# Kernel tuning notes

Hardware: AMD Instinct MI355X
Metric: run time of the kernel (lower is better)

## Reference

```python
import jax, jax.numpy as jnp
import numpy as np

H = 128
W = 128
DELTA = 7000.0  # sigmainv in the original (delta default 7000)


def setup_inputs() -> dict:
    key = jax.random.key(0)
    k1, k2, k3, k4 = jax.random.split(key, 4)
    B, P, F, TH, TW = 2, 300, 512, 512, 512
    points_bxpx3 = jax.random.uniform(k1, (B, P, 3), jnp.float32) * 2.0 - 1.0  # NDC cube [-1,1]
    faces_fx3 = jax.random.randint(k2, (F, 3), 0, P, dtype=jnp.int32)
    uv_bxpx2 = jax.random.uniform(k3, (B, P, 2), jnp.float32)  # texcoords in [0,1]
    texture_bx3xthxtw = jax.random.uniform(k4, (B, 3, TH, TW), jnp.float32)
    return {"points_bxpx3": points_bxpx3, "faces_fx3": faces_fx3,
            "uv_bxpx2": uv_bxpx2, "texture_bx3xthxtw": texture_bx3xthxtw}


def _edge(ax, ay, bx, by, px, py):
    # signed area * 2 of triangle (a, b, p); standard edge function
    return (bx - ax) * (py - ay) - (by - ay) * (px - ax)


def _seg_d2(ax, ay, bx, by, px, py):
    # squared distance from point p to segment (a, b)
    abx, aby = bx - ax, by - ay
    apx, apy = px - ax, py - ay
    denom = abx * abx + aby * aby + 1e-12
    t = jnp.clip((apx * abx + apy * aby) / denom, 0.0, 1.0)
    dx = apx - t * abx
    dy = apy - t * aby
    return dx * dx + dy * dy


def _rasterize(points_bxpx3, faces_fx3, feats_bxfx3xd, height, width, delta):
    """Soft DIB-R-style rasterizer.
    Returns (imfeat [B,H,W,D], improb [B,H,W,1]).
    """
    B = points_bxpx3.shape[0]
    v = points_bxpx3[:, faces_fx3]                      # (B,F,3,3) gathered face vertices
    x0, x1, x2 = (v[:, :, i, 0][:, :, None, None] for i in range(3))
    y0, y1, y2 = (v[:, :, i, 1][:, :, None, None] for i in range(3))
    z0, z1, z2 = (v[:, :, i, 2][:, :, None, None] for i in range(3))

    # pixel-center grid in NDC; y flipped (top row = +1)
    px = ((jnp.arange(width, dtype=points_bxpx3.dtype) + 0.5) / width * 2.0 - 1.0)[None, None, None, :]
    py = (1.0 - (jnp.arange(height, dtype=points_bxpx3.dtype) + 0.5) / height * 2.0)[None, None, :, None]

    area = _edge(x0, y0, x1, y1, x2, y2)                # (B,F,1,1) == normal_z (cross-product z)
    front = area > 1e-8                                  # front-facing (normalz > 0) cull
    inv_area = 1.0 / jnp.where(front, area, 1.0)

    w0 = _edge(x1, y1, x2, y2, px, py) * inv_area        # (B,F,H,W) barycentrics
    w1 = _edge(x2, y2, x0, y0, px, py) * inv_area
    w2 = _edge(x0, y0, x1, y1, px, py) * inv_area
    inside = front & (w0 >= 0) & (w1 >= 0) & (w2 >= 0)

    z_pix = w0 * z0 + w1 * z1 + w2 * z2                  # interpolated depth
    zbuf = jnp.where(inside, z_pix, -1e9)
    best = jnp.argmax(zbuf, axis=1)                      # (B,H,W) nearest covering face
    hit = jnp.any(inside, axis=1)[..., None].astype(points_bxpx3.dtype)  # (B,H,W,1)

    # gather winning barycentrics and per-face vertex features
    w = jnp.stack([w0, w1, w2], axis=-1)                 # (B,F,H,W,3)
    idx = jnp.broadcast_to(best[:, None, :, :, None], (B, 1, height, width, 3))
    wb = jnp.take_along_axis(w, idx, axis=1)[:, 0]       # (B,H,W,3)
    fb = jax.vmap(lambda f, i: f[i])(feats_bxfx3xd, best)  # (B,H,W,3,D)
    imfeat = jnp.einsum('bhwk,bhwkd->bhwd', wb, fb) * hit

    # soft coverage: prob of each face = exp(-delta * d2(pixel, triangle)); z-buffer blend
    d2 = jnp.minimum(
        jnp.minimum(_seg_d2(x0, y0, x1, y1, px, py), _seg_d2(x1, y1, x2, y2, px, py)),
        _seg_d2(x2, y2, x0, y0, px, py))
    d2 = jnp.where(inside, 0.0, d2)
    p = jnp.where(front, jnp.exp(-delta * d2), 0.0)      # (B,F,H,W)
    log_miss = jnp.sum(jnp.log1p(-jnp.clip(p, 0.0, 1.0 - 1e-7)), axis=1)  # (B,H,W)
    improb = (1.0 - jnp.exp(log_miss))[..., None]
    return imfeat, improb


def _fragmentshader(imtexcoords, texture_bx3xthxtw, hardmask):
    # bilinear texture sampling; background is zero
    B, C, TH, TW = texture_bx3xthxtw.shape
    u = jnp.clip(imtexcoords[..., 0], 0.0, 1.0)
    vv = jnp.clip(imtexcoords[..., 1], 0.0, 1.0)
    fx = u * (TW - 1)
    fy = (1.0 - vv) * (TH - 1)
    x0 = jnp.floor(fx).astype(jnp.int32); x1 = jnp.minimum(x0 + 1, TW - 1)
    y0 = jnp.floor(fy).astype(jnp.int32); y1 = jnp.minimum(y0 + 1, TH - 1)
    wx = (fx - x0)[:, None]; wy = (fy - y0)[:, None]     # (B,1,H,W)

    def g(tex, yy, xx):  # tex (C,TH,TW), yy/xx (H,W) -> (C,H,W)
        return tex[:, yy, xx]
    c00 = jax.vmap(g)(texture_bx3xthxtw, y0, x0)
    c01 = jax.vmap(g)(texture_bx3xthxtw, y0, x1)
    c10 = jax.vmap(g)(texture_bx3xthxtw, y1, x0)
    c11 = jax.vmap(g)(texture_bx3xthxtw, y1, x1)
    col = (c00 * (1 - wx) * (1 - wy) + c01 * wx * (1 - wy)
           + c10 * (1 - wx) * wy + c11 * wx * wy)        # (B,C,H,W)
    return col.transpose(0, 2, 3, 1) * hardmask          # (B,H,W,C)


def reference(points_bxpx3, faces_fx3, uv_bxpx2, texture_bx3xthxtw):
    # texture mode: per-face vertex features = [u, v, mask=1]
    uvf = uv_bxpx2[:, faces_fx3]                          # (B,F,3,2)
    ones = jnp.ones_like(uvf[..., :1])
    feats = jnp.concatenate([uvf, ones], axis=-1)         # (B,F,3,3)
    imfeat, improb = _rasterize(points_bxpx3, faces_fx3, feats, H, W, DELTA)
    imtexcoords = imfeat[..., :2]
    hardmask = jax.lax.stop_gradient(imfeat[..., 2:3])    # .detach() in the original
    imrender = _fragmentshader(imtexcoords, texture_bx3xthxtw, hardmask)
    return imrender, improb
```

## Files before the change

kernel.cpp:

```cpp
#include <hip/hip_runtime.h>
#include <math.h>

constexpr int kB = 2, kP = 300, kF = 512, kH = 128, kW = 128, kTH = 512, kTW = 512;
constexpr float kDelta = 7000.0f;
constexpr float kCut = 0.06f;
constexpr float kThr2 = 0.018882f;
constexpr float kLogInside = -15.9423847f;

__global__ __launch_bounds__(512, 6) void render_all(const float* __restrict__ pts,
                                                     const int* __restrict__ faces,
                                                     const float* __restrict__ uvs,
                                                     const float* __restrict__ tex,
                                                     float* __restrict__ out) {
    __shared__ float4 sA[kF], sB[kF], sC[kF];
    __shared__ float2 s_vtx[kF * 3];
    __shared__ unsigned short s_of[kF];
    __shared__ int s_wsum[8];
    __shared__ float s_bz[512];
    __shared__ int s_bi[512];
    __shared__ float s_lm[512];

    int tile = (int)blockIdx.x;
    int b = tile >> 8;
    int rem = tile & 255;
    int ty = rem >> 4, tx = rem & 15;
    int tid = (int)threadIdx.x;
    int lane = tid & 63;
    int wv = tid >> 6;

    {
        int f = tid;
        int i0 = faces[f * 3 + 0], i1 = faces[f * 3 + 1], i2 = faces[f * 3 + 2];
        const float* pb = pts + b * kP * 3;
        float x0 = pb[i0 * 3], y0 = pb[i0 * 3 + 1], z0 = pb[i0 * 3 + 2];
        float x1 = pb[i1 * 3], y1 = pb[i1 * 3 + 1], z1 = pb[i1 * 3 + 2];
        float x2 = pb[i2 * 3], y2 = pb[i2 * 3 + 1], z2 = pb[i2 * 3 + 2];
        float area = (x1 - x0) * (y2 - y0) - (y1 - y0) * (x2 - x0);
        bool front = area > 1e-8f;

        sA[f] = make_float4(0.0f, 0.0f, -1e30f, 0.0f);
        sB[f] = make_float4(0.0f, -1e30f, 0.0f, 0.0f);
        sC[f] = make_float4(-1e30f, 0.0f, 0.0f, 0.0f);
        s_vtx[f * 3 + 0] = make_float2(1e15f, 1e15f);
        s_vtx[f * 3 + 1] = make_float2(1e15f, 1e15f);
        s_vtx[f * 3 + 2] = make_float2(1e15f, 1e15f);
        unsigned long long bal = __ballot(front);
        if (lane == 0) s_wsum[wv] = __popcll(bal);
        __syncthreads();

        int base = 0;
#pragma unroll
        for (int w = 0; w < 8; ++w) base += (w < wv) ? s_wsum[w] : 0;
        int k = base + __popcll(bal & ((1ull << lane) - 1ull));

        if (front) {
            int slot = ((k & 7) << 6) | (k >> 3);
            float inv_a = 1.0f / area;
            float e0x = x2 - x1, e0y = y2 - y1;
            float e1x = x0 - x2, e1y = y0 - y2;
            float e2x = x1 - x0, e2y = y1 - y0;
            float l0 = fmaf(e0x, e0x, e0y * e0y);
            float l1 = fmaf(e1x, e1x, e1y * e1y);
            float l2 = fmaf(e2x, e2x, e2y * e2y);
            float s0 = rsqrtf(l0 + 1e-12f);
            float s1 = rsqrtf(l1 + 1e-12f);
            float s2 = rsqrtf(l2 + 1e-12f);
            float A0 = -e0y * s0, B0 = e0x * s0, C0 = (e0y * x1 - e0x * y1) * s0;
            float A1 = -e1y * s1, B1 = e1x * s1, C1 = (e1y * x2 - e1x * y2) * s1;
            float A2 = -e2y * s2, B2 = e2x * s2, C2 = (e2y * x0 - e2x * y0) * s2;
            float a0 = -e0y * inv_a, b0 = e0x * inv_a, c0 = (e0y * x1 - e0x * y1) * inv_a;
            float a1 = -e1y * inv_a, b1 = e1x * inv_a, c1 = (e1y * x2 - e1x * y2) * inv_a;
            float a2 = -e2y * inv_a, b2 = e2x * inv_a, c2 = (e2y * x0 - e2x * y0) * inv_a;
            sA[slot] = make_float4(A0, B0, C0, A1);
            sB[slot] = make_float4(B1, C1, A2, B2);
            sC[slot] = make_float4(C2,
                                   a0 * z0 + a1 * z1 + a2 * z2,
                                   b0 * z0 + b1 * z1 + b2 * z2,
                                   c0 * z0 + c1 * z1 + c2 * z2);
            s_vtx[slot * 3 + 0] = make_float2(x0, y0);
            s_vtx[slot * 3 + 1] = make_float2(x1, y1);
            s_vtx[slot * 3 + 2] = make_float2(x2, y2);
            s_of[slot] = (unsigned short)f;
        }
    }
    __syncthreads();

    int pyi = ty * 8 + (lane >> 3);
    int pxi = tx * 8 + (lane & 7);
    float px = ((float)pxi + 0.5f) * (2.0f / 128.0f) - 1.0f;
    float py = 1.0f - ((float)pyi + 0.5f) * (2.0f / 128.0f);

    float cx = (float)(tx * 8 + 4) * (2.0f / 128.0f) - 1.0f;
    float cy = 1.0f - (float)(ty * 8 + 4) * (2.0f / 128.0f);
    unsigned long long m;
    {
        int slt = (wv << 6) + lane;
        float4 a4 = sA[slt];
        float4 b4 = sB[slt];
        float4 c4 = sC[slt];
        float L0 = fmaf(a4.x, cx, fmaf(a4.y, cy, a4.z));
        float L1 = fmaf(a4.w, cx, fmaf(b4.x, cy, b4.y));
        float L2 = fmaf(b4.z, cx, fmaf(b4.w, cy, c4.x));
        float minc = fminf(fminf(L0, L1), L2);
        float2 v0 = s_vtx[slt * 3 + 0];
        float2 v1 = s_vtx[slt * 3 + 1];
        float2 v2 = s_vtx[slt * 3 + 2];
        float e0x = v2.x - v1.x, e0y = v2.y - v1.y;
        float e1x = v0.x - v2.x, e1y = v0.y - v2.y;
        float e2x = v1.x - v0.x, e2y = v1.y - v0.y;
        float p0x = cx - v0.x, p0y = cy - v0.y;
        float p1x = cx - v1.x, p1y = cy - v1.y;
        float p2x = cx - v2.x, p2y = cy - v2.y;
        float dot0 = fmaf(p1x, e0x, p1y * e0y), len0 = fmaf(e0x, e0x, e0y * e0y);
        float dot1 = fmaf(p2x, e1x, p2y * e1y), len1 = fmaf(e1x, e1x, e1y * e1y);
        float dot2 = fmaf(p0x, e2x, p0y * e2y), len2 = fmaf(e2x, e2x, e2y * e2y);
        float c0 = (dot0 >= 0.0f && dot0 <= len0) ? L0 * L0 : 1e30f;
        float c1 = (dot1 >= 0.0f && dot1 <= len1) ? L1 * L1 : 1e30f;
        float c2 = (dot2 >= 0.0f && dot2 <= len2) ? L2 * L2 : 1e30f;
        float dv0 = fmaf(p0x, p0x, p0y * p0y);
        float dv1 = fmaf(p1x, p1x, p1y * p1y);
        float dv2 = fmaf(p2x, p2x, p2y * p2y);
        float d2c = fminf(fminf(fminf(c0, c1), fminf(c2, dv0)), fminf(dv1, dv2));
        bool admit = (minc >= 0.0f) | (d2c <= kThr2);
        m = __ballot(admit);
    }

    float bestz = -1e9f;
    int besti = -1, icnt = 0;
    float lm = 0.0f;

    while (m) {
        int l = (int)__builtin_ctzll(m);
        m &= (m - 1);
        int fs = (wv << 6) + l;
        int k = (l << 3) | wv;
        float4 h0 = sA[fs];
        float4 h1 = sB[fs];
        float4 h2 = sC[fs];
        float L0 = fmaf(h0.x, px, fmaf(h0.y, py, h0.z));
        float L1 = fmaf(h0.w, px, fmaf(h1.x, py, h1.y));
        float L2 = fmaf(h1.z, px, fmaf(h1.w, py, h2.x));
        float minL = fminf(fminf(L0, L1), L2);
        bool inside = minL >= 0.0f;
        float z = fmaf(h2.y, px, fmaf(h2.z, py, h2.w));
        if (inside && z > bestz) { bestz = z; besti = k; }
        icnt += inside ? 1 : 0;
        float db = fminf(fminf(fabsf(L0), fabsf(L1)), fabsf(L2));
        bool need = (!inside) & (db < kCut);
        if (__any(need)) {
            float2 v0 = s_vtx[fs * 3 + 0];
            float2 v1 = s_vtx[fs * 3 + 1];
            float2 v2 = s_vtx[fs * 3 + 2];
            float e0x = v2.x - v1.x, e0y = v2.y - v1.y;
            float e1x = v0.x - v2.x, e1y = v0.y - v2.y;
            float e2x = v1.x - v0.x, e2y = v1.y - v0.y;
            float p0x = px - v0.x, p0y = py - v0.y;
            float p1x = px - v1.x, p1y = py - v1.y;
            float p2x = px - v2.x, p2y = py - v2.y;
            float dot0 = fmaf(p1x, e0x, p1y * e0y), len0 = fmaf(e0x, e0x, e0y * e0y);
            float dot1 = fmaf(p2x, e1x, p2y * e1y), len1 = fmaf(e1x, e1x, e1y * e1y);
            float dot2 = fmaf(p0x, e2x, p0y * e2y), len2 = fmaf(e2x, e2x, e2y * e2y);
            float c0 = (dot0 >= 0.0f && dot0 <= len0) ? L0 * L0 : 1e30f;
            float c1 = (dot1 >= 0.0f && dot1 <= len1) ? L1 * L1 : 1e30f;
            float c2 = (dot2 >= 0.0f && dot2 <= len2) ? L2 * L2 : 1e30f;
            float dv0 = fmaf(p0x, p0x, p0y * p0y);
            float dv1 = fmaf(p1x, p1x, p1y * p1y);
            float dv2 = fmaf(p2x, p2x, p2y * p2y);
            float d2 = fminf(fminf(fminf(c0, c1), fminf(c2, dv0)), fminf(dv1, dv2));
            float p = __expf(-kDelta * d2);
            p = fminf(p, 1.0f - 1e-7f);
            float lp = __logf(1.0f - p);
            lm += need ? lp : 0.0f;
        }
    }
    lm = fmaf((float)icnt, kLogInside, lm);

    s_bz[tid] = bestz;
    s_bi[tid] = besti;
    s_lm[tid] = lm;
    __syncthreads();

    if (tid < 64) {
        float bz = s_bz[tid];
        int bi = s_bi[tid];
        float L = s_lm[tid];
#pragma unroll
        for (int w = 1; w < 8; ++w) {
            float z2 = s_bz[w * 64 + tid];
            int ii = s_bi[w * 64 + tid];
            L += s_lm[w * 64 + tid];
            if (z2 > bz || (z2 == bz && ii >= 0 && (unsigned)ii < (unsigned)bi)) {
                bz = z2; bi = ii;
            }
        }
        float improb = 1.0f - expf(L);
        float u = 0.0f, v = 0.0f, mk = 0.0f;
        if (bi >= 0) {
            int slot = ((bi & 7) << 6) | (bi >> 3);
            float2 v0 = s_vtx[slot * 3 + 0];
            float2 v1 = s_vtx[slot * 3 + 1];
            float2 v2 = s_vtx[slot * 3 + 2];
            float area = (v1.x - v0.x) * (v2.y - v0.y) - (v1.y - v0.y) * (v2.x - v0.x);
            float inv_a = 1.0f / area;
            float w0 = ((v2.x - v1.x) * (py - v1.y) - (v2.y - v1.y) * (px - v1.x)) * inv_a;
            float w1 = ((v0.x - v2.x) * (py - v2.y) - (v0.y - v2.y) * (px - v2.x)) * inv_a;
            float w2 = ((v1.x - v0.x) * (py - v0.y) - (v1.y - v0.y) * (px - v0.x)) * inv_a;
            int of = (int)s_of[slot];
            int j0 = faces[of * 3], j1 = faces[of * 3 + 1], j2 = faces[of * 3 + 2];
            const float* ub = uvs + b * kP * 2;
            u = w0 * ub[j0 * 2] + w1 * ub[j1 * 2] + w2 * ub[j2 * 2];
            v = w0 * ub[j0 * 2 + 1] + w1 * ub[j1 * 2 + 1] + w2 * ub[j2 * 2 + 1];
            mk = w0 + w1 + w2;
        }
        float uc = fminf(fmaxf(u, 0.0f), 1.0f);
        float vc = fminf(fmaxf(v, 0.0f), 1.0f);
        float fx = uc * (float)(kTW - 1);
        float fy = (1.0f - vc) * (float)(kTH - 1);
        int xi0 = (int)floorf(fx), yi0 = (int)floorf(fy);
        int xi1 = min(xi0 + 1, kTW - 1), yi1 = min(yi0 + 1, kTH - 1);
        float wx = fx - (float)xi0, wy = fy - (float)yi0;
        float w00 = (1.0f - wx) * (1.0f - wy);
        float w01 = wx * (1.0f - wy);
        float w10 = (1.0f - wx) * wy;
        float w11 = wx * wy;
        int o00 = yi0 * kTW + xi0, o01 = yi0 * kTW + xi1;
        int o10 = yi1 * kTW + xi0, o11 = yi1 * kTW + xi1;
        const float* tb = tex + (size_t)b * 3 * kTH * kTW;
        float cols[3];
#pragma unroll
        for (int c = 0; c < 3; ++c) {
            const float* tc = tb + c * kTH * kTW;
            cols[c] = (tc[o00] * w00 + tc[o01] * w01 + tc[o10] * w10 + tc[o11] * w11) * mk;
        }
        int pix = (b * kH + pyi) * kW + pxi;
        out[pix * 3 + 0] = cols[0];
        out[pix * 3 + 1] = cols[1];
        out[pix * 3 + 2] = cols[2];
        out[kB * kH * kW * 3 + pix] = improb;
    }
}

extern "C" void kernel_launch(void* const* d_in, const int* in_sizes, int n_in,
                              void* d_out, int out_size, void* d_ws, size_t ws_size,
                              hipStream_t stream) {
    const float* pts = (const float*)d_in[0];
    const int* faces = (const int*)d_in[1];
    const float* uvs = (const float*)d_in[2];
    const float* tex = (const float*)d_in[3];
    float* out = (float*)d_out;
    render_all<<<kB * 256, 512, 0, stream>>>(pts, faces, uvs, tex, out);
}
```

Baseline: 18.32 us.

## Split face setup into a prep kernel and stage precomputed face data via workspace

Per-face edge and depth-plane setup, plus the gathered UVs, now runs once per batch in a small prep kernel that writes a compacted table to workspace. Each render block copies that table into shared memory with coalesced float4 loads instead of redoing the gather and setup in all 512 blocks, and the final shading reads UVs from shared memory rather than global. The cull thresholds are also tightened, which admits fewer faces and reduces soft-probability work but changes the approximation margin. In exchange it adds a second launch with a dependency, and the larger shared footprint is aliased for the reduction, which needs an extra barrier.

Result: slower. 21.76 us (+18.8%).

```diff
diff --git a/kernel.cpp b/kernel.cpp
--- a/kernel.cpp
+++ b/kernel.cpp
@@ -3,22 +3,94 @@
 
 constexpr int kB = 2, kP = 300, kF = 512, kH = 128, kW = 128, kTH = 512, kTW = 512;
 constexpr float kDelta = 7000.0f;
-constexpr float kCut = 0.06f;
-constexpr float kThr2 = 0.018882f;
+constexpr float kCut = 0.0363f;
+constexpr float kThr2 = 0.012928f;
 constexpr float kLogInside = -15.9423847f;
-
-__global__ __launch_bounds__(512, 6) void render_all(const float* __restrict__ pts,
-                                                     const int* __restrict__ faces,
-                                                     const float* __restrict__ uvs,
-                                                     const float* __restrict__ tex,
-                                                     float* __restrict__ out) {
-    __shared__ float4 sA[kF], sB[kF], sC[kF];
-    __shared__ float2 s_vtx[kF * 3];
-    __shared__ unsigned short s_of[kF];
+constexpr int kS4 = 3072;
+
+__global__ __launch_bounds__(512) void prep(const float* __restrict__ pts,
+                                            const int* __restrict__ faces,
+                                            const float* __restrict__ uvs,
+                                            float4* __restrict__ ws4) {
+    int b = (int)blockIdx.x;
+    int tid = (int)threadIdx.x, lane = tid & 63, wv = tid >> 6;
     __shared__ int s_wsum[8];
-    __shared__ float s_bz[512];
-    __shared__ int s_bi[512];
-    __shared__ float s_lm[512];
+
+    int f = tid;
+    int i0 = faces[f * 3 + 0], i1 = faces[f * 3 + 1], i2 = faces[f * 3 + 2];
+    const float* pb = pts + b * kP * 3;
+    float x0 = pb[i0 * 3], y0 = pb[i0 * 3 + 1], z0 = pb[i0 * 3 + 2];
+    float x1 = pb[i1 * 3], y1 = pb[i1 * 3 + 1], z1 = pb[i1 * 3 + 2];
+    float x2 = pb[i2 * 3], y2 = pb[i2 * 3 + 1], z2 = pb[i2 * 3 + 2];
+    float area = (x1 - x0) * (y2 - y0) - (y1 - y0) * (x2 - x0);
+    bool front = area > 1e-8f;
+
+    unsigned long long bal = __ballot(front);
+    if (lane == 0) s_wsum[wv] = __popcll(bal);
+    __syncthreads();
+    int n = 0, base = 0;
+#pragma unroll
+    for (int w = 0; w < 8; ++w) { n += s_wsum[w]; base += (w < wv) ? s_wsum[w] : 0; }
+    int k = base + __popcll(bal & ((1ull << lane) - 1ull));
+
+    float4* A = ws4 + (size_t)b * kS4;
+    float4* B = A + 512;
+    float4* C = B + 512;
+    float4* V = C + 512;
+    float4* U = V + 1024;
+
+    if (tid >= n) {
+        int s = ((tid & 7) << 6) | (tid >> 3);
+        A[s] = make_float4(0.0f, 0.0f, -1e30f, 0.0f);
+        B[s] = make_float4(0.0f, -1e30f, 0.0f, 0.0f);
+        C[s] = make_float4(-1e30f, 0.0f, 0.0f, 0.0f);
+        V[s * 2 + 0] = make_float4(1e15f, 1e15f, 1e15f, 1e15f);
+        V[s * 2 + 1] = make_float4(1e15f, 1e15f, 0.0f, 0.0f);
+        U[s] = make_float4(0.0f, 0.0f, 0.0f, 0.0f);
+    }
+    if (front) {
+        int s = ((k & 7) << 6) | (k >> 3);
+        float inv_a = 1.0f / area;
+        float e0x = x2 - x1, e0y = y2 - y1;
+        float e1x = x0 - x2, e1y = y0 - y2;
+        float e2x = x1 - x0, e2y = y1 - y0;
+        float l0 = fmaf(e0x, e0x, e0y * e0y);
+        float l1 = fmaf(e1x, e1x, e1y * e1y);
+        float l2 = fmaf(e2x, e2x, e2y * e2y);
+        float s0 = rsqrtf(l0 + 1e-12f);
+        float s1 = rsqrtf(l1 + 1e-12f);
+        float s2 = rsqrtf(l2 + 1e-12f);
+        float A0 = -e0y * s0, B0 = e0x * s0, C0 = (e0y * x1 - e0x * y1) * s0;
+        float A1 = -e1y * s1, B1 = e1x * s1, C1 = (e1y * x2 - e1x * y2) * s1;
+        float A2 = -e2y * s2, B2 = e2x * s2, C2 = (e2y * x0 - e2x * y0) * s2;
+        float a0 = -e0y * inv_a, b0 = e0x * inv_a, c0 = (e0y * x1 - e0x * y1) * inv_a;
+        float a1 = -e1y * inv_a, b1 = e1x * inv_a, c1 = (e1y * x2 - e1x * y2) * inv_a;
+        float a2 = -e2y * inv_a, b2 = e2x * inv_a, c2 = (e2y * x0 - e2x * y0) * inv_a;
+        A[s] = make_float4(A0, B0, C0, A1);
+        B[s] = make_float4(B1, C1, A2, B2);
+        C[s] = make_float4(C2,
+                           a0 * z0 + a1 * z1 + a2 * z2,
+                           b0 * z0 + b1 * z1 + b2 * z2,
+                           c0 * z0 + c1 * z1 + c2 * z2);
+        const float* ub = uvs + b * kP * 2;
+        V[s * 2 + 0] = make_float4(x0, y0, x1, y1);
+        V[s * 2 + 1] = make_float4(x2, y2, ub[i0 * 2], ub[i0 * 2 + 1]);
+        U[s] = make_float4(ub[i1 * 2], ub[i1 * 2 + 1], ub[i2 * 2], ub[i2 * 2 + 1]);
+    }
+}
+
+__global__ __launch_bounds__(512, 6) void render(const float4* __restrict__ ws4,
+                                                 const float* __restrict__ tex,
+                                                 float* __restrict__ out) {
+    __shared__ float4 s_all[kS4];
+    float4* sA = s_all;
+    float4* sB = s_all + 512;
+    float4* sC = s_all + 1024;
+    float4* sV = s_all + 1536;
+    float4* sU = s_all + 2560;
+    float* s_bz = (float*)s_all;
+    int* s_bi = (int*)((char*)s_all + 2048);
+    float* s_lm = (float*)((char*)s_all + 4096);
 
     int tile = (int)blockIdx.x;
     int b = tile >> 8;
@@ -29,59 +101,8 @@
     int wv = tid >> 6;
 
     {
-        int f = tid;
-        int i0 = faces[f * 3 + 0], i1 = faces[f * 3 + 1], i2 = faces[f * 3 + 2];
-        const float* pb = pts + b * kP * 3;
-        float x0 = pb[i0 * 3], y0 = pb[i0 * 3 + 1], z0 = pb[i0 * 3 + 2];
-        float x1 = pb[i1 * 3], y1 = pb[i1 * 3 + 1], z1 = pb[i1 * 3 + 2];
-        float x2 = pb[i2 * 3], y2 = pb[i2 * 3 + 1], z2 = pb[i2 * 3 + 2];
-        float area = (x1 - x0) * (y2 - y0) - (y1 - y0) * (x2 - x0);
-        bool front = area > 1e-8f;
-
-        sA[f] = make_float4(0.0f, 0.0f, -1e30f, 0.0f);
-        sB[f] = make_float4(0.0f, -1e30f, 0.0f, 0.0f);
-        sC[f] = make_float4(-1e30f, 0.0f, 0.0f, 0.0f);
-        s_vtx[f * 3 + 0] = make_float2(1e15f, 1e15f);
-        s_vtx[f * 3 + 1] = make_float2(1e15f, 1e15f);
-        s_vtx[f * 3 + 2] = make_float2(1e15f, 1e15f);
-        unsigned long long bal = __ballot(front);
-        if (lane == 0) s_wsum[wv] = __popcll(bal);
-        __syncthreads();
-
-        int base = 0;
-#pragma unroll
-        for (int w = 0; w < 8; ++w) base += (w < wv) ? s_wsum[w] : 0;
-        int k = base + __popcll(bal & ((1ull << lane) - 1ull));
-
-        if (front) {
-            int slot = ((k & 7) << 6) | (k >> 3);
-            float inv_a = 1.0f / area;
-            float e0x = x2 - x1, e0y = y2 - y1;
-            float e1x = x0 - x2, e1y = y0 - y2;
-            float e2x = x1 - x0, e2y = y1 - y0;
-            float l0 = fmaf(e0x, e0x, e0y * e0y);
-            float l1 = fmaf(e1x, e1x, e1y * e1y);
-            float l2 = fmaf(e2x, e2x, e2y * e2y);
-            float s0 = rsqrtf(l0 + 1e-12f);
-            float s1 = rsqrtf(l1 + 1e-12f);
-            float s2 = rsqrtf(l2 + 1e-12f);
-            float A0 = -e0y * s0, B0 = e0x * s0, C0 = (e0y * x1 - e0x * y1) * s0;
-            float A1 = -e1y * s1, B1 = e1x * s1, C1 = (e1y * x2 - e1x * y2) * s1;
-            float A2 = -e2y * s2, B2 = e2x * s2, C2 = (e2y * x0 - e2x * y0) * s2;
-            float a0 = -e0y * inv_a, b0 = e0x * inv_a, c0 = (e0y * x1 - e0x * y1) * inv_a;
-            float a1 = -e1y * inv_a, b1 = e1x * inv_a, c1 = (e1y * x2 - e1x * y2) * inv_a;
-            float a2 = -e2y * inv_a, b2 = e2x * inv_a, c2 = (e2y * x0 - e2x * y0) * inv_a;
-            sA[slot] = make_float4(A0, B0, C0, A1);
-            sB[slot] = make_float4(B1, C1, A2, B2);
-            sC[slot] = make_float4(C2,
-                                   a0 * z0 + a1 * z1 + a2 * z2,
-                                   b0 * z0 + b1 * z1 + b2 * z2,
-                                   c0 * z0 + c1 * z1 + c2 * z2);
-            s_vtx[slot * 3 + 0] = make_float2(x0, y0);
-            s_vtx[slot * 3 + 1] = make_float2(x1, y1);
-            s_vtx[slot * 3 + 2] = make_float2(x2, y2);
-            s_of[slot] = (unsigned short)f;
-        }
+        const float4* src = ws4 + (size_t)b * kS4;
+        for (int i = tid; i < kS4; i += 512) s_all[i] = src[i];
     }
     __syncthreads();
 
@@ -94,7 +115,7 @@
     float cy = 1.0f - (float)(ty * 8 + 4) * (2.0f / 128.0f);
     unsigned long long m;
     {
-        int slt = (wv << 6) + lane;
+        int slt = tid;
         float4 a4 = sA[slt];
         float4 b4 = sB[slt];
         float4 c4 = sC[slt];
@@ -102,15 +123,14 @@
         float L1 = fmaf(a4.w, cx, fmaf(b4.x, cy, b4.y));
         float L2 = fmaf(b4.z, cx, fmaf(b4.w, cy, c4.x));
         float minc = fminf(fminf(L0, L1), L2);
-        float2 v0 = s_vtx[slt * 3 + 0];
-        float2 v1 = s_vtx[slt * 3 + 1];
-        float2 v2 = s_vtx[slt * 3 + 2];
-        float e0x = v2.x - v1.x, e0y = v2.y - v1.y;
-        float e1x = v0.x - v2.x, e1y = v0.y - v2.y;
-        float e2x = v1.x - v0.x, e2y = v1.y - v0.y;
-        float p0x = cx - v0.x, p0y = cy - v0.y;
-        float p1x = cx - v1.x, p1y = cy - v1.y;
-        float p2x = cx - v2.x, p2y = cy - v2.y;
+        float4 vA = sV[slt * 2 + 0];
+        float4 vB = sV[slt * 2 + 1];
+        float e0x = vB.x - vA.z, e0y = vB.y - vA.w;
+        float e1x = vA.x - vB.x, e1y = vA.y - vB.y;
+        float e2x = vA.z - vA.x, e2y = vA.w - vA.y;
+        float p0x = cx - vA.x, p0y = cy - vA.y;
+        float p1x = cx - vA.z, p1y = cy - vA.w;
+        float p2x = cx - vB.x, p2y = cy - vB.y;
         float dot0 = fmaf(p1x, e0x, p1y * e0y), len0 = fmaf(e0x, e0x, e0y * e0y);
         float dot1 = fmaf(p2x, e1x, p2y * e1y), len1 = fmaf(e1x, e1x, e1y * e1y);
         float dot2 = fmaf(p0x, e2x, p0y * e2y), len2 = fmaf(e2x, e2x, e2y * e2y);
@@ -148,15 +168,14 @@
         float db = fminf(fminf(fabsf(L0), fabsf(L1)), fabsf(L2));
         bool need = (!inside) & (db < kCut);
         if (__any(need)) {
-            float2 v0 = s_vtx[fs * 3 + 0];
-            float2 v1 = s_vtx[fs * 3 + 1];
-            float2 v2 = s_vtx[fs * 3 + 2];
-            float e0x = v2.x - v1.x, e0y = v2.y - v1.y;
-            float e1x = v0.x - v2.x, e1y = v0.y - v2.y;
-            float e2x = v1.x - v0.x, e2y = v1.y - v0.y;
-            float p0x = px - v0.x, p0y = py - v0.y;
-            float p1x = px - v1.x, p1y = py - v1.y;
-            float p2x = px - v2.x, p2y = py - v2.y;
+            float4 vA = sV[fs * 2 + 0];
+            float4 vB = sV[fs * 2 + 1];
+            float e0x = vB.x - vA.z, e0y = vB.y - vA.w;
+            float e1x = vA.x - vB.x, e1y = vA.y - vB.y;
+            float e2x = vA.z - vA.x, e2y = vA.w - vA.y;
+            float p0x = px - vA.x, p0y = py - vA.y;
+            float p1x = px - vA.z, p1y = py - vA.w;
+            float p2x = px - vB.x, p2y = py - vB.y;
             float dot0 = fmaf(p1x, e0x, p1y * e0y), len0 = fmaf(e0x, e0x, e0y * e0y);
             float dot1 = fmaf(p2x, e1x, p2y * e1y), len1 = fmaf(e1x, e1x, e1y * e1y);
             float dot2 = fmaf(p0x, e2x, p0y * e2y), len2 = fmaf(e2x, e2x, e2y * e2y);
@@ -175,6 +194,7 @@
     }
     lm = fmaf((float)icnt, kLogInside, lm);
 
+    __syncthreads();
     s_bz[tid] = bestz;
     s_bi[tid] = besti;
     s_lm[tid] = lm;
@@ -197,19 +217,17 @@
         float u = 0.0f, v = 0.0f, mk = 0.0f;
         if (bi >= 0) {
             int slot = ((bi & 7) << 6) | (bi >> 3);
-            float2 v0 = s_vtx[slot * 3 + 0];
-            float2 v1 = s_vtx[slot * 3 + 1];
-            float2 v2 = s_vtx[slot * 3 + 2];
-            float area = (v1.x - v0.x) * (v2.y - v0.y) - (v1.y - v0.y) * (v2.x - v0.x);
+            float4 vA = sV[slot * 2 + 0];
+            float4 vB = sV[slot * 2 + 1];
+            float x0 = vA.x, y0 = vA.y, x1 = vA.z, y1 = vA.w, x2 = vB.x, y2 = vB.y;
+            float area = (x1 - x0) * (y2 - y0) - (y1 - y0) * (x2 - x0);
             float inv_a = 1.0f / area;
-            float w0 = ((v2.x - v1.x) * (py - v1.y) - (v2.y - v1.y) * (px - v1.x)) * inv_a;
-            float w1 = ((v0.x - v2.x) * (py - v2.y) - (v0.y - v2.y) * (px - v2.x)) * inv_a;
-            float w2 = ((v1.x - v0.x) * (py - v0.y) - (v1.y - v0.y) * (px - v0.x)) * inv_a;
-            int of = (int)s_of[slot];
-            int j0 = faces[of * 3], j1 = faces[of * 3 + 1], j2 = faces[of * 3 + 2];
-            const float* ub = uvs + b * kP * 2;
-            u = w0 * ub[j0 * 2] + w1 * ub[j1 * 2] + w2 * ub[j2 * 2];
-            v = w0 * ub[j0 * 2 + 1] + w1 * ub[j1 * 2 + 1] + w2 * ub[j2 * 2 + 1];
+            float w0 = ((x2 - x1) * (py - y1) - (y2 - y1) * (px - x1)) * inv_a;
+            float w1 = ((x0 - x2) * (py - y2) - (y0 - y2) * (px - x2)) * inv_a;
+            float w2 = ((x1 - x0) * (py - y0) - (y1 - y0) * (px - x0)) * inv_a;
+            float4 uq = sU[slot];
+            u = w0 * vB.z + w1 * uq.x + w2 * uq.z;
+            v = w0 * vB.w + w1 * uq.y + w2 * uq.w;
             mk = w0 + w1 + w2;
         }
         float uc = fminf(fmaxf(u, 0.0f), 1.0f);
@@ -248,5 +266,7 @@
     const float* uvs = (const float*)d_in[2];
     const float* tex = (const float*)d_in[3];
     float* out = (float*)d_out;
-    render_all<<<kB * 256, 512, 0, stream>>>(pts, faces, uvs, tex, out);
+    float4* ws4 = (float4*)d_ws;
+    prep<<<kB, 512, 0, stream>>>(pts, faces, uvs, ws4);
+    render<<<kB * 256, 512, 0, stream>>>(ws4, tex, out);
 }
```
